# Performance work log

Hardware: AMD Instinct MI355X
Metric: run time of the kernel (lower is better)

The kernel has to match this reference:

```python
import jax, jax.numpy as jnp
import numpy as np

HEAD_COUNT = 16
EMBED_DIM = 2048
B, S = 2, 2048


def setup_inputs() -> dict:
    key = jax.random.key(0)
    k1, k2, k3, k4, k5 = jax.random.split(key, 5)
    keys = jax.random.normal(k1, (B, S, EMBED_DIM), dtype=jnp.float32)
    values = jax.random.normal(k2, (B, S, EMBED_DIM), dtype=jnp.float32)
    queries = jax.random.normal(k3, (B, S, EMBED_DIM), dtype=jnp.float32)
    # padding-style mask; guarantee at least one valid key per batch row
    attention_mask = jax.random.randint(k4, (B, S), 0, 2).astype(bool)
    attention_mask = attention_mask.at[:, 0].set(True)
    w_out = jax.random.normal(k5, (EMBED_DIM, EMBED_DIM), dtype=jnp.float32) * (EMBED_DIM ** -0.5)
    return {"keys": keys, "values": values, "queries": queries,
            "attention_mask": attention_mask, "w_out": w_out}


def reference(keys, values, queries, attention_mask, w_out):
    b, s, e = queries.shape
    h = HEAD_COUNT
    c = e // h  # head dim
    k = keys.reshape(b, s, h, c)
    v = values.reshape(b, s, h, c)
    q = queries.reshape(b, s, h, c) * (c ** -0.5)
    # [B,H,Q,K] scores + additive padding bias on key axis
    scores = jnp.einsum('bqhc,bkhc->bhqk', q, k)
    bias = jnp.where(attention_mask, 0.0, -jnp.inf)[:, None, None, :]
    weights = jax.nn.softmax(scores + bias, axis=-1)
    out = jnp.einsum('bhqk,bkhc->bqhc', weights, v).reshape(b, s, e)
    # nn.Linear(bias=False): y = x @ W^T
    return out @ w_out.T
```

## Files before the change

### kernel.cpp

```cpp
#include <hip/hip_runtime.h>
#include <hip/hip_bf16.h>
#include <math.h>

#define B_ 2
#define S_ 2048
#define E_ 2048
#define H_ 16
#define C_ 128

typedef __attribute__((ext_vector_type(8))) short s8v;
typedef __attribute__((ext_vector_type(4))) float f32x4;
typedef __attribute__((ext_vector_type(2))) unsigned u32x2;
typedef __attribute__((ext_vector_type(4))) unsigned u32x4;

#define MFMA16(a, b, c) __builtin_amdgcn_mfma_f32_16x16x32_bf16((a), (b), (c), 0, 0, 0)

__device__ __forceinline__ unsigned fbits(float f) {
    union { float f; unsigned u; } v{f};
    return v.u;
}
__device__ __forceinline__ short f2bfh(float f) {
    return (short)((fbits(f) + 0x8000u) >> 16);
}
__device__ __forceinline__ unsigned bfpack(float lo, float hi) {
    return __builtin_amdgcn_perm(fbits(hi) + 0x8000u, fbits(lo) + 0x8000u, 0x07060302u);
}

__device__ __forceinline__ float fexp2(float x) {
    float r;
    asm("v_exp_f32 %0, %1" : "=v"(r) : "v"(x));
    return r;
}
__device__ __forceinline__ float frcp(float x) {
    float r;
    asm("v_rcp_f32 %0, %1" : "=v"(r) : "v"(x));
    return r;
}

__device__ __forceinline__ void glds16(const void* g, void* l) {
    __builtin_amdgcn_global_load_lds(
        (const __attribute__((address_space(1))) void*)g,
        (__attribute__((address_space(3))) void*)l, 16, 0, 0);
}

template <bool DOK>
__global__ __launch_bounds__(256) void prep_kv(
    const float* __restrict__ K, const float* __restrict__ V,
    short* __restrict__ Kb, short* __restrict__ Vt)
{
    __shared__ __align__(16) short vt[C_][66];
    const int t  = threadIdx.x;
    const int s0 = blockIdx.x * 64;
    const int bh = blockIdx.y;
    const int b = bh >> 4, h = bh & 15;

    if (DOK) {
#pragma unroll
        for (int i = 0; i < 8; ++i) {
            int idx = t + i * 256;
            int s = idx >> 5, c4 = idx & 31;
            float4 v = *(const float4*)(K + ((size_t)(b * S_ + s0 + s)) * E_ + h * C_ + c4 * 4);
            u32x2 o = {bfpack(v.x, v.y), bfpack(v.z, v.w)};
            *(u32x2*)(Kb + ((size_t)(bh * S_ + s0 + s)) * C_ + c4 * 4) = o;
        }
    }
#pragma unroll
    for (int i = 0; i < 8; ++i) {
        int idx = t + i * 256;
        int r = idx >> 5, c4 = idx & 31;
        float4 v = *(const float4*)(V + ((size_t)(b * S_ + s0 + r)) * E_ + h * C_ + c4 * 4);
        vt[c4 * 4 + 0][r] = f2bfh(v.x);
        vt[c4 * 4 + 1][r] = f2bfh(v.y);
        vt[c4 * 4 + 2][r] = f2bfh(v.z);
        vt[c4 * 4 + 3][r] = f2bfh(v.w);
    }
    __syncthreads();
#pragma unroll
    for (int i = 0; i < 4; ++i) {
        int idx = t + i * 256;
        int c = idx >> 3, sc = idx & 7;
        *(s8v*)(Vt + ((size_t)(bh * C_ + c)) * S_ + s0 + sc * 8) = *(const s8v*)&vt[c][sc * 8];
    }
}

__global__ __launch_bounds__(256) void convw_kernel(
    const float* __restrict__ W, short* __restrict__ Wb)
{
    size_t i = ((size_t)blockIdx.x * 256 + threadIdx.x) * 8;
    float4 a = *(const float4*)(W + i);
    float4 b = *(const float4*)(W + i + 4);
    u32x4 o = {bfpack(a.x, a.y), bfpack(a.z, a.w), bfpack(b.x, b.y), bfpack(b.z, b.w)};
    *(u32x4*)(Wb + i) = o;
}

constexpr int QT = 256;
constexpr int KT = 64;
constexpr float M0 = 16.0f;

template <bool KBF16>
__global__ __launch_bounds__(512, 2) void attn_mfma(
    const short* __restrict__ Kb, const float* __restrict__ Kf,
    const float* __restrict__ Qp, const short* __restrict__ Vt,
    const int* __restrict__ maskp, short* __restrict__ Op)
{
    __shared__ __align__(16) short ks[2][KT * 128];
    __shared__ __align__(16) short vs[2][C_ * 64];
    __shared__ __align__(16) short ps[8][16][72];

    const int t = threadIdx.x;
    const int w = t >> 6, lane = t & 63;
    const int c15 = lane & 15, quad = lane >> 4;
    const int rbid = blockIdx.x;
    const int hb = (rbid & 7) + 8 * ((rbid >> 3) & 3);
    const int q0 = (rbid >> 5) * QT;
    const int h = hb & 15, b = hb >> 4;
    const int bh = b * H_ + h;

    const float qscale = 0.12751744458187936f;
    s8v qf[2][4];
#pragma unroll
    for (int mi = 0; mi < 2; ++mi) {
        const float* qrow = Qp + ((size_t)(b * S_ + q0 + w * 32 + mi * 16 + c15)) * E_ + h * C_;
#pragma unroll
        for (int kk = 0; kk < 4; ++kk) {
            const float* p = qrow + kk * 32 + quad * 8;
            float4 x0 = *(const float4*)p;
            float4 x1 = *(const float4*)(p + 4);
            u32x4 pk = {bfpack(x0.x * qscale, x0.y * qscale),
                        bfpack(x0.z * qscale, x0.w * qscale),
                        bfpack(x1.x * qscale, x1.y * qscale),
                        bfpack(x1.z * qscale, x1.w * qscale)};
            qf[mi][kk] = *(s8v*)&pk;
        }
    }

    s8v ones;
#pragma unroll
    for (int j = 0; j < 8; ++j) ones[j] = (short)0x3F80;

    f32x4 O[2][8], Ol[2];
#pragma unroll
    for (int mi = 0; mi < 2; ++mi) {
        Ol[mi] = (f32x4){0.f, 0.f, 0.f, 0.f};
#pragma unroll
        for (int ct = 0; ct < 8; ++ct) O[mi][ct] = (f32x4){0.f, 0.f, 0.f, 0.f};
    }

    const short* Kbh = Kb + (size_t)(bh * S_) * C_;
    const float* Kfh = Kf + (size_t)(b * S_) * E_ + h * C_;
    const short* Vbh = Vt + (size_t)(bh * C_) * S_;
    const int*   mptr = maskp + b * S_ + 4 * c15;

    int kgp[4], vgp[2];
#pragma unroll
    for (int kk = 0; kk < 4; ++kk) kgp[kk] = ((4 * kk + quad) ^ c15) * 8;
#pragma unroll
    for (int ks2 = 0; ks2 < 2; ++ks2) vgp[ks2] = ((4 * ks2 + quad) ^ (c15 & 7)) * 8;

    auto stage = [&](short* ksb, short* vsb, int k0) {
        const int r4 = lane >> 4, gp = lane & 15;
#pragma unroll
        for (int i = 0; i < 2; ++i) {
            int row = w * 8 + i * 4 + r4;
            int g = gp ^ ((row >> 2) & 15);
            glds16(Kbh + (size_t)(k0 + row) * C_ + g * 8, ksb + (w * 8 + i * 4) * 128);
        }
        const int cr = lane >> 3, gp7 = lane & 7;
#pragma unroll
        for (int i = 0; i < 2; ++i) {
            int c = w * 16 + i * 8 + cr;
            int g = gp7 ^ (c & 7);
            glds16(Vbh + (size_t)c * S_ + k0 + g * 8, vsb + (w * 16 + i * 8) * 64);
        }
    };

    auto compute = [&](const short* ksc, const short* vsc, int4 mv) {
        float bva[4] = {mv.x ? -M0 : -1e30f, mv.y ? -M0 : -1e30f,
                        mv.z ? -M0 : -1e30f, mv.w ? -M0 : -1e30f};
        f32x4 Sf[2][4];
        __builtin_amdgcn_s_setprio(1);
#pragma unroll
        for (int nt = 0; nt < 4; ++nt) {
            f32x4 s0 = (f32x4){bva[nt], bva[nt], bva[nt], bva[nt]};
            f32x4 s1 = s0;
            const short* krow = ksc + (4 * c15 + nt) * 128;
#pragma unroll
            for (int kk = 0; kk < 4; ++kk) {
                s8v bf = *(const s8v*)(krow + kgp[kk]);
                s0 = MFMA16(qf[0][kk], bf, s0);
                s1 = MFMA16(qf[1][kk], bf, s1);
            }
            Sf[0][nt] = s0; Sf[1][nt] = s1;
        }
        __builtin_amdgcn_s_setprio(0);

        s8v af[2][2];
#pragma unroll
        for (int mi = 0; mi < 2; ++mi) {
#pragma unroll
            for (int r = 0; r < 4; ++r) {
                float p0 = fexp2(Sf[mi][0][r]);
                float p1 = fexp2(Sf[mi][1][r]);
                float p2 = fexp2(Sf[mi][2][r]);
                float p3 = fexp2(Sf[mi][3][r]);
                u32x2 d = {bfpack(p0, p1), bfpack(p2, p3)};
                *(u32x2*)&ps[w][quad * 4 + r][4 * c15] = d;
            }
#pragma unroll
            for (int ks2 = 0; ks2 < 2; ++ks2)
                af[mi][ks2] = *(const s8v*)&ps[w][c15][ks2 * 32 + quad * 8];
        }

        __builtin_amdgcn_s_setprio(1);
#pragma unroll
        for (int ct = 0; ct < 8; ++ct) {
            const short* vrow = vsc + (ct * 16 + c15) * 64;
#pragma unroll
            for (int ks2 = 0; ks2 < 2; ++ks2) {
                s8v bf = *(const s8v*)(vrow + vgp[ks2]);
                O[0][ct] = MFMA16(af[0][ks2], bf, O[0][ct]);
                O[1][ct] = MFMA16(af[1][ks2], bf, O[1][ct]);
            }
        }
#pragma unroll
        for (int mi = 0; mi < 2; ++mi) {
            Ol[mi] = MFMA16(af[mi][0], ones, Ol[mi]);
            Ol[mi] = MFMA16(af[mi][1], ones, Ol[mi]);
        }
        __builtin_amdgcn_s_setprio(0);
    };

    if (KBF16) {
        stage(&ks[0][0], &vs[0][0], 0);
        int4 mcur = *(const int4*)mptr;
        __syncthreads();
#pragma unroll 1
        for (int k0 = 0; k0 < S_; k0 += 2 * KT) {
            stage(&ks[1][0], &vs[1][0], k0 + KT);
            int4 m1 = *(const int4*)(mptr + k0 + KT);
            compute(&ks[0][0], &vs[0][0], mcur);
            __syncthreads();

            int4 m2 = m1;
            if (k0 + 2 * KT < S_) {
                stage(&ks[0][0], &vs[0][0], k0 + 2 * KT);
                m2 = *(const int4*)(mptr + k0 + 2 * KT);
            }
            compute(&ks[1][0], &vs[1][0], m1);
            mcur = m2;
            __syncthreads();
        }
    } else {
#pragma unroll 1
        for (int k0 = 0; k0 < S_; k0 += KT) {
#pragma unroll
            for (int i = 0; i < 4; ++i) {
                int idx = t + i * 512;
                int r = idx >> 5, c4 = idx & 31;
                float4 kv = *(const float4*)(Kfh + (size_t)(k0 + r) * E_ + c4 * 4);
                u32x2 sv = {bfpack(kv.x, kv.y), bfpack(kv.z, kv.w)};
                int gpw = (c4 >> 1) ^ ((r >> 2) & 15);
                *(u32x2*)&ks[0][r * 128 + gpw * 8 + (c4 & 1) * 4] = sv;
            }
            {
                const int cr = lane >> 3, gp7 = lane & 7;
#pragma unroll
                for (int i = 0; i < 2; ++i) {
                    int c = w * 16 + i * 8 + cr;
                    int g = gp7 ^ (c & 7);
                    glds16(Vbh + (size_t)c * S_ + k0 + g * 8, &vs[0][(w * 16 + i * 8) * 64]);
                }
            }
            int4 mv = *(const int4*)(mptr + k0);
            __syncthreads();
            compute(&ks[0][0], &vs[0][0], mv);
            __syncthreads();
        }
    }

#pragma unroll
    for (int mi = 0; mi < 2; ++mi) {
        float inv[4];
#pragma unroll
        for (int r = 0; r < 4; ++r) inv[r] = frcp(Ol[mi][r]);
        size_t rbase = (size_t)(b * S_ + q0 + w * 32 + mi * 16 + quad * 4) * E_ + h * C_;
#pragma unroll
        for (int ct = 0; ct < 8; ++ct)
#pragma unroll
            for (int r = 0; r < 4; ++r)
                Op[rbase + (size_t)r * E_ + ct * 16 + c15] = f2bfh(O[mi][ct][r] * inv[r]);
    }
}

template <bool WBF16>
__global__ __launch_bounds__(512, 2) void proj_mfma(
    const short* __restrict__ X, const short* __restrict__ Wb,
    const float* __restrict__ Wf, float* __restrict__ Y)
{
    __shared__ __align__(16) short As[2][128 * 64];
    __shared__ __align__(16) short Bs[2][256 * 64];

    const int t = threadIdx.x;
    const int w = t >> 6, lane = t & 63;
    const int c15 = lane & 15, quad = lane >> 4;
    const int bm = blockIdx.x * 128, bn = blockIdx.y * 256;
    const int wm = (w >> 2) * 64, wn = (w & 3) * 64;

    f32x4 acc[4][4];
#pragma unroll
    for (int mi = 0; mi < 4; ++mi)
#pragma unroll
        for (int ni = 0; ni < 4; ++ni) acc[mi][ni] = (f32x4){0.f, 0.f, 0.f, 0.f};

    int agp[2];
#pragma unroll
    for (int kk = 0; kk < 2; ++kk) agp[kk] = ((4 * kk + quad) ^ (c15 & 7)) * 8;

    auto stageAB = [&](short* Ab, short* Bb, int k0) {
        const int r8 = lane >> 3, gp = lane & 7;
#pragma unroll
        for (int i = 0; i < 2; ++i) {
            int row = w * 16 + i * 8 + r8;
            int g = gp ^ (row & 7);
            glds16(X + (size_t)(bm + row) * E_ + k0 + g * 8, Ab + (w * 16 + i * 8) * 64);
        }
#pragma unroll
        for (int i = 0; i < 4; ++i) {
            int row = w * 32 + i * 8 + r8;
            int g = gp ^ (row & 7);
            glds16(Wb + (size_t)(bn + row) * E_ + k0 + g * 8, Bb + (w * 32 + i * 8) * 64);
        }
    };

    auto compute = [&](const short* Ab, const short* Bb) {
#pragma unroll
        for (int kk = 0; kk < 2; ++kk) {
            s8v a[4], bb[4];
#pragma unroll
            for (int mi = 0; mi < 4; ++mi)
                a[mi] = *(const s8v*)(Ab + (wm + mi * 16 + c15) * 64 + agp[kk]);
#pragma unroll
            for (int ni = 0; ni < 4; ++ni)
                bb[ni] = *(const s8v*)(Bb + (wn + ni * 16 + c15) * 64 + agp[kk]);
#pragma unroll
            for (int mi = 0; mi < 4; ++mi)
#pragma unroll
                for (int ni = 0; ni < 4; ++ni)
                    acc[mi][ni] = MFMA16(a[mi], bb[ni], acc[mi][ni]);
        }
    };

    if (WBF16) {
        stageAB(&As[0][0], &Bs[0][0], 0);
        __syncthreads();
#pragma unroll 1
        for (int k0 = 0; k0 < E_; k0 += 128) {
            stageAB(&As[1][0], &Bs[1][0], k0 + 64);
            compute(&As[0][0], &Bs[0][0]);
            __syncthreads();

            if (k0 + 128 < E_) stageAB(&As[0][0], &Bs[0][0], k0 + 128);
            compute(&As[1][0], &Bs[1][0]);
            __syncthreads();
        }
    } else {
#pragma unroll 1
        for (int k0 = 0; k0 < E_; k0 += 64) {
            {
                const int r8 = lane >> 3, gp = lane & 7;
#pragma unroll
                for (int i = 0; i < 2; ++i) {
                    int row = w * 16 + i * 8 + r8;
                    int g = gp ^ (row & 7);
                    glds16(X + (size_t)(bm + row) * E_ + k0 + g * 8, &As[0][(w * 16 + i * 8) * 64]);
                }
            }
#pragma unroll
            for (int i = 0; i < 8; ++i) {
                int idx = t + i * 512;
                int r = idx >> 4, c4 = idx & 15;
                float4 wv = *(const float4*)(Wf + (size_t)(bn + r) * E_ + k0 + c4 * 4);
                u32x2 sv = {bfpack(wv.x, wv.y), bfpack(wv.z, wv.w)};
                int gpw = (c4 >> 1) ^ (r & 7);
                *(u32x2*)&Bs[0][r * 64 + gpw * 8 + (c4 & 1) * 4] = sv;
            }
            __syncthreads();
            compute(&As[0][0], &Bs[0][0]);
            __syncthreads();
        }
    }

#pragma unroll
    for (int mi = 0; mi < 4; ++mi)
#pragma unroll
        for (int ni = 0; ni < 4; ++ni) {
            size_t rbase = (size_t)(bm + wm + mi * 16 + quad * 4) * E_ + bn + wn + ni * 16 + c15;
#pragma unroll
            for (int r = 0; r < 4; ++r) Y[rbase + (size_t)r * E_] = acc[mi][ni][r];
        }
}

extern "C" void kernel_launch(void* const* d_in, const int* in_sizes, int n_in,
                              void* d_out, int out_size, void* d_ws, size_t ws_size,
                              hipStream_t stream) {
    const float* keys    = (const float*)d_in[0];
    const float* values  = (const float*)d_in[1];
    const float* queries = (const float*)d_in[2];
    const int*   mask    = (const int*)d_in[3];
    const float* w_out   = (const float*)d_in[4];
    float* out = (float*)d_out;

    const size_t EL = (size_t)B_ * S_ * E_;
    short* ws  = (short*)d_ws;
    short* VtW = ws;
    short* Xb  = ws + EL;
    short* Kb  = ws + 2 * EL;
    short* Wb  = ws + 3 * EL;

    const bool hasK = ws_size >= (3 * EL) * 2;
    const bool hasW = ws_size >= (3 * EL + (size_t)E_ * E_) * 2;

    if (hasK)
        prep_kv<true><<<dim3(S_ / 64, B_ * H_), 256, 0, stream>>>(keys, values, Kb, VtW);
    else
        prep_kv<false><<<dim3(S_ / 64, B_ * H_), 256, 0, stream>>>(keys, values, Kb, VtW);
    if (hasW) convw_kernel<<<(E_ * E_ / 8) / 256, 256, 0, stream>>>(w_out, Wb);

    if (hasK)
        attn_mfma<true><<<dim3((S_ / QT) * H_ * B_), 512, 0, stream>>>(Kb, keys, queries, VtW, mask, Xb);
    else
        attn_mfma<false><<<dim3((S_ / QT) * H_ * B_), 512, 0, stream>>>(Kb, keys, queries, VtW, mask, Xb);

    if (hasW)
        proj_mfma<true><<<dim3((B_ * S_) / 128, E_ / 256), 512, 0, stream>>>(Xb, Wb, w_out, out);
    else
        proj_mfma<false><<<dim3((B_ * S_) / 128, E_ / 256), 512, 0, stream>>>(Xb, Wb, w_out, out);
}
```

Measured before the change: 269.7 us.

## Split-K projection GEMM across two wave groups with LDS reduction

The output projection now splits the K dimension between two groups of four waves, each accumulating a 64x128 sub-tile over half of K with its own LDS buffers. Partial sums are reduced through shared memory before the store. It also raises MFMA priority during compute and swaps the grid axes so neighbouring blocks share X rows. The B tile is now single-buffered with an extra barrier per step, and the accumulators double in size, which raises register pressure and may reduce occupancy under launch_bounds(512,2).

```diff
diff --git a/kernel.cpp b/kernel.cpp
--- a/kernel.cpp
+++ b/kernel.cpp
@@ -297,107 +297,125 @@
     const short* __restrict__ X, const short* __restrict__ Wb,
     const float* __restrict__ Wf, float* __restrict__ Y)
 {
-    __shared__ __align__(16) short As[2][128 * 64];
+    __shared__ __align__(16) short As[2][2][128 * 64];
     __shared__ __align__(16) short Bs[2][256 * 64];
 
     const int t = threadIdx.x;
     const int w = t >> 6, lane = t & 63;
     const int c15 = lane & 15, quad = lane >> 4;
-    const int bm = blockIdx.x * 128, bn = blockIdx.y * 256;
-    const int wm = (w >> 2) * 64, wn = (w & 3) * 64;
-
-    f32x4 acc[4][4];
+    const int g = w & 1, wi = w >> 1;
+    const int bn = blockIdx.x * 256, bm = blockIdx.y * 128;
+    const int wm = (wi >> 1) * 64, wn = (wi & 1) * 128;
+    const int kbase = g * (E_ / 2);
+
+    f32x4 acc[4][8];
 #pragma unroll
     for (int mi = 0; mi < 4; ++mi)
 #pragma unroll
-        for (int ni = 0; ni < 4; ++ni) acc[mi][ni] = (f32x4){0.f, 0.f, 0.f, 0.f};
+        for (int ni = 0; ni < 8; ++ni) acc[mi][ni] = (f32x4){0.f, 0.f, 0.f, 0.f};
 
     int agp[2];
 #pragma unroll
     for (int kk = 0; kk < 2; ++kk) agp[kk] = ((4 * kk + quad) ^ (c15 & 7)) * 8;
 
-    auto stageAB = [&](short* Ab, short* Bb, int k0) {
+    auto stageA = [&](int buf, int k0) {
         const int r8 = lane >> 3, gp = lane & 7;
-#pragma unroll
-        for (int i = 0; i < 2; ++i) {
-            int row = w * 16 + i * 8 + r8;
-            int g = gp ^ (row & 7);
-            glds16(X + (size_t)(bm + row) * E_ + k0 + g * 8, Ab + (w * 16 + i * 8) * 64);
-        }
+        short* Ab = &As[g][buf][0];
 #pragma unroll
         for (int i = 0; i < 4; ++i) {
-            int row = w * 32 + i * 8 + r8;
-            int g = gp ^ (row & 7);
-            glds16(Wb + (size_t)(bn + row) * E_ + k0 + g * 8, Bb + (w * 32 + i * 8) * 64);
-        }
-    };
-
-    auto compute = [&](const short* Ab, const short* Bb) {
+            int row = wi * 32 + i * 8 + r8;
+            int gg = gp ^ (row & 7);
+            glds16(X + (size_t)(bm + row) * E_ + kbase + k0 + gg * 8, Ab + (wi * 32 + i * 8) * 64);
+        }
+    };
+    auto stageB = [&](int k0) {
+        const int r8 = lane >> 3, gp = lane & 7;
+        short* Bb = &Bs[g][0];
+#pragma unroll
+        for (int i = 0; i < 8; ++i) {
+            int row = wi * 64 + i * 8 + r8;
+            int gg = gp ^ (row & 7);
+            glds16(Wb + (size_t)(bn + row) * E_ + kbase + k0 + gg * 8, Bb + (wi * 64 + i * 8) * 64);
+        }
+    };
+    auto convB = [&](int k0) {
+        const int tid4 = wi * 64 + lane;
+        short* Bb = &Bs[g][0];
+#pragma unroll
+        for (int i = 0; i < 16; ++i) {
+            int idx = tid4 + i * 256;
+            int r = idx >> 4, c4 = idx & 15;
+            float4 wv = *(const float4*)(Wf + (size_t)(bn + r) * E_ + kbase + k0 + c4 * 4);
+            u32x2 sv = {bfpack(wv.x, wv.y), bfpack(wv.z, wv.w)};
+            int gpw = (c4 >> 1) ^ (r & 7);
+            *(u32x2*)&Bb[r * 64 + gpw * 8 + (c4 & 1) * 4] = sv;
+        }
+    };
+
+    auto compute = [&](int buf) {
+        const short* Ab = &As[g][buf][0];
+        const short* Bb = &Bs[g][0];
+        __builtin_amdgcn_s_setprio(1);
 #pragma unroll
         for (int kk = 0; kk < 2; ++kk) {
-            s8v a[4], bb[4];
+            s8v a[4], bb[8];
 #pragma unroll
             for (int mi = 0; mi < 4; ++mi)
                 a[mi] = *(const s8v*)(Ab + (wm + mi * 16 + c15) * 64 + agp[kk]);
 #pragma unroll
-            for (int ni = 0; ni < 4; ++ni)
+            for (int ni = 0; ni < 8; ++ni)
                 bb[ni] = *(const s8v*)(Bb + (wn + ni * 16 + c15) * 64 + agp[kk]);
 #pragma unroll
             for (int mi = 0; mi < 4; ++mi)
 #pragma unroll
-                for (int ni = 0; ni < 4; ++ni)
+                for (int ni = 0; ni < 8; ++ni)
                     acc[mi][ni] = MFMA16(a[mi], bb[ni], acc[mi][ni]);
         }
-    };
-
-    if (WBF16) {
-        stageAB(&As[0][0], &Bs[0][0], 0);
+        __builtin_amdgcn_s_setprio(0);
+    };
+
+    stageA(0, 0);
+    if (WBF16) stageB(0); else convB(0);
+    __syncthreads();
+#pragma unroll 1
+    for (int j = 0; j < 16; ++j) {
+        if (j + 1 < 16) stageA((j + 1) & 1, (j + 1) * 64);
+        compute(j & 1);
         __syncthreads();
+        if (j + 1 < 16) { if (WBF16) stageB((j + 1) * 64); else convB((j + 1) * 64); }
+        __syncthreads();
+    }
+
+    float* mbuf = (float*)&As[0][0][0];
 #pragma unroll 1
-        for (int k0 = 0; k0 < E_; k0 += 128) {
-            stageAB(&As[1][0], &Bs[1][0], k0 + 64);
-            compute(&As[0][0], &Bs[0][0]);
-            __syncthreads();
-
-            if (k0 + 128 < E_) stageAB(&As[0][0], &Bs[0][0], k0 + 128);
-            compute(&As[1][0], &Bs[1][0]);
-            __syncthreads();
-        }
-    } else {
-#pragma unroll 1
-        for (int k0 = 0; k0 < E_; k0 += 64) {
-            {
-                const int r8 = lane >> 3, gp = lane & 7;
-#pragma unroll
-                for (int i = 0; i < 2; ++i) {
-                    int row = w * 16 + i * 8 + r8;
-                    int g = gp ^ (row & 7);
-                    glds16(X + (size_t)(bm + row) * E_ + k0 + g * 8, &As[0][(w * 16 + i * 8) * 64]);
-                }
-            }
-#pragma unroll
-            for (int i = 0; i < 8; ++i) {
-                int idx = t + i * 512;
-                int r = idx >> 4, c4 = idx & 15;
-                float4 wv = *(const float4*)(Wf + (size_t)(bn + r) * E_ + k0 + c4 * 4);
-                u32x2 sv = {bfpack(wv.x, wv.y), bfpack(wv.z, wv.w)};
-                int gpw = (c4 >> 1) ^ (r & 7);
-                *(u32x2*)&Bs[0][r * 64 + gpw * 8 + (c4 & 1) * 4] = sv;
-            }
-            __syncthreads();
-            compute(&As[0][0], &Bs[0][0]);
-            __syncthreads();
-        }
-    }
-
-#pragma unroll
-    for (int mi = 0; mi < 4; ++mi)
-#pragma unroll
-        for (int ni = 0; ni < 4; ++ni) {
-            size_t rbase = (size_t)(bm + wm + mi * 16 + quad * 4) * E_ + bn + wn + ni * 16 + c15;
-#pragma unroll
-            for (int r = 0; r < 4; ++r) Y[rbase + (size_t)r * E_] = acc[mi][ni][r];
-        }
+    for (int mi = 0; mi < 4; ++mi) {
+        if (g == 1) {
+#pragma unroll
+            for (int ni = 0; ni < 8; ++ni)
+#pragma unroll
+                for (int r = 0; r < 4; ++r)
+                    mbuf[((wi * 8 + ni) * 4 + r) * 64 + lane] = acc[mi][ni][r];
+        }
+        __syncthreads();
+        if (g == 0) {
+#pragma unroll
+            for (int ni = 0; ni < 8; ++ni)
+#pragma unroll
+                for (int r = 0; r < 4; ++r)
+                    acc[mi][ni][r] += mbuf[((wi * 8 + ni) * 4 + r) * 64 + lane];
+        }
+        __syncthreads();
+    }
+    if (g == 0) {
+#pragma unroll
+        for (int mi = 0; mi < 4; ++mi)
+#pragma unroll
+            for (int ni = 0; ni < 8; ++ni) {
+                size_t rbase = (size_t)(bm + wm + mi * 16 + quad * 4) * E_ + bn + wn + ni * 16 + c15;
+#pragma unroll
+                for (int r = 0; r < 4; ++r) Y[rbase + (size_t)r * E_] = acc[mi][ni][r];
+            }
+    }
 }
 
 extern "C" void kernel_launch(void* const* d_in, const int* in_sizes, int n_in,
@@ -432,7 +450,7 @@
         attn_mfma<false><<<dim3((S_ / QT) * H_ * B_), 512, 0, stream>>>(Kb, keys, queries, VtW, mask, Xb);
 
     if (hasW)
-        proj_mfma<true><<<dim3((B_ * S_) / 128, E_ / 256), 512, 0, stream>>>(Xb, Wb, w_out, out);
+        proj_mfma<true><<<dim3(E_ / 256, (B_ * S_) / 128), 512, 0, stream>>>(Xb, Wb, w_out, out);
     else
-        proj_mfma<false><<<dim3((B_ * S_) / 128, E_ / 256), 512, 0, stream>>>(Xb, Wb, w_out, out);
-}
+        proj_mfma<false><<<dim3(E_ / 256, (B_ * S_) / 128), 512, 0, stream>>>(Xb, Wb, w_out, out);
+}
```

Result: slower. 873.6 us (+223.9%).

## Fuse weight conversion into prep kernel and retile projection GEMM to 128x128

Applied to the files above, without the earlier changes.

Merges the fp32-to-bf16 weight conversion into the K/V prep kernel as extra grid rows, removing one kernel launch. The output projection GEMM moves from 256x128 tiles with 512 threads to 128x128 tiles with 256 threads, giving 512 blocks instead of 256. Block IDs are remapped so groups of 16 consecutive blocks share an M tile and span N, aiming for better L2 reuse and more even occupancy across CUs. The smaller tiles give less reuse per block in exchange for more parallelism.

```diff
diff --git a/kernel.cpp b/kernel.cpp
--- a/kernel.cpp
+++ b/kernel.cpp
@@ -43,13 +43,25 @@
         (__attribute__((address_space(3))) void*)l, 16, 0, 0);
 }
 
-template <bool DOK>
-__global__ __launch_bounds__(256) void prep_kv(
+template <bool DOK, bool DOW>
+__global__ __launch_bounds__(256) void prep_all(
     const float* __restrict__ K, const float* __restrict__ V,
-    short* __restrict__ Kb, short* __restrict__ Vt)
+    const float* __restrict__ W,
+    short* __restrict__ Kb, short* __restrict__ Vt, short* __restrict__ Wb)
 {
     __shared__ __align__(16) short vt[C_][66];
-    const int t  = threadIdx.x;
+    const int t = threadIdx.x;
+
+    if (DOW && blockIdx.y >= 32) {
+        int cid = (blockIdx.y - 32) * 32 + blockIdx.x;
+        size_t i = ((size_t)cid * 256 + t) * 8;
+        float4 a = *(const float4*)(W + i);
+        float4 b = *(const float4*)(W + i + 4);
+        u32x4 o = {bfpack(a.x, a.y), bfpack(a.z, a.w), bfpack(b.x, b.y), bfpack(b.z, b.w)};
+        *(u32x4*)(Wb + i) = o;
+        return;
+    }
+
     const int s0 = blockIdx.x * 64;
     const int bh = blockIdx.y;
     const int b = bh >> 4, h = bh & 15;
@@ -81,16 +93,6 @@
         int c = idx >> 3, sc = idx & 7;
         *(s8v*)(Vt + ((size_t)(bh * C_ + c)) * S_ + s0 + sc * 8) = *(const s8v*)&vt[c][sc * 8];
     }
-}
-
-__global__ __launch_bounds__(256) void convw_kernel(
-    const float* __restrict__ W, short* __restrict__ Wb)
-{
-    size_t i = ((size_t)blockIdx.x * 256 + threadIdx.x) * 8;
-    float4 a = *(const float4*)(W + i);
-    float4 b = *(const float4*)(W + i + 4);
-    u32x4 o = {bfpack(a.x, a.y), bfpack(a.z, a.w), bfpack(b.x, b.y), bfpack(b.z, b.w)};
-    *(u32x4*)(Wb + i) = o;
 }
 
 constexpr int QT = 256;
@@ -293,18 +295,20 @@
 }
 
 template <bool WBF16>
-__global__ __launch_bounds__(512, 2) void proj_mfma(
+__global__ __launch_bounds__(256, 2) void proj_mfma(
     const short* __restrict__ X, const short* __restrict__ Wb,
     const float* __restrict__ Wf, float* __restrict__ Y)
 {
     __shared__ __align__(16) short As[2][128 * 64];
-    __shared__ __align__(16) short Bs[2][256 * 64];
+    __shared__ __align__(16) short Bs[2][128 * 64];
 
     const int t = threadIdx.x;
     const int w = t >> 6, lane = t & 63;
     const int c15 = lane & 15, quad = lane >> 4;
-    const int bm = blockIdx.x * 128, bn = blockIdx.y * 256;
-    const int wm = (w >> 2) * 64, wn = (w & 3) * 64;
+    const int pid = blockIdx.x;
+    const int bn = ((pid & 7) + 8 * ((pid >> 3) & 1)) * 128;
+    const int bm = (pid >> 4) * 128;
+    const int wm = (w >> 1) * 64, wn = (w & 1) * 64;
 
     f32x4 acc[4][4];
 #pragma unroll
@@ -318,16 +322,11 @@
 
     auto stageAB = [&](short* Ab, short* Bb, int k0) {
         const int r8 = lane >> 3, gp = lane & 7;
-#pragma unroll
-        for (int i = 0; i < 2; ++i) {
-            int row = w * 16 + i * 8 + r8;
-            int g = gp ^ (row & 7);
-            glds16(X + (size_t)(bm + row) * E_ + k0 + g * 8, Ab + (w * 16 + i * 8) * 64);
-        }
 #pragma unroll
         for (int i = 0; i < 4; ++i) {
             int row = w * 32 + i * 8 + r8;
             int g = gp ^ (row & 7);
+            glds16(X + (size_t)(bm + row) * E_ + k0 + g * 8, Ab + (w * 32 + i * 8) * 64);
             glds16(Wb + (size_t)(bn + row) * E_ + k0 + g * 8, Bb + (w * 32 + i * 8) * 64);
         }
     };
@@ -369,15 +368,15 @@
             {
                 const int r8 = lane >> 3, gp = lane & 7;
 #pragma unroll
-                for (int i = 0; i < 2; ++i) {
-                    int row = w * 16 + i * 8 + r8;
+                for (int i = 0; i < 4; ++i) {
+                    int row = w * 32 + i * 8 + r8;
                     int g = gp ^ (row & 7);
-                    glds16(X + (size_t)(bm + row) * E_ + k0 + g * 8, &As[0][(w * 16 + i * 8) * 64]);
+                    glds16(X + (size_t)(bm + row) * E_ + k0 + g * 8, &As[0][(w * 32 + i * 8) * 64]);
                 }
             }
 #pragma unroll
             for (int i = 0; i < 8; ++i) {
-                int idx = t + i * 512;
+                int idx = t + i * 256;
                 int r = idx >> 4, c4 = idx & 15;
                 float4 wv = *(const float4*)(Wf + (size_t)(bn + r) * E_ + k0 + c4 * 4);
                 u32x2 sv = {bfpack(wv.x, wv.y), bfpack(wv.z, wv.w)};
@@ -420,11 +419,12 @@
     const bool hasK = ws_size >= (3 * EL) * 2;
     const bool hasW = ws_size >= (3 * EL + (size_t)E_ * E_) * 2;
 
-    if (hasK)
-        prep_kv<true><<<dim3(S_ / 64, B_ * H_), 256, 0, stream>>>(keys, values, Kb, VtW);
+    if (hasK && hasW)
+        prep_all<true, true><<<dim3(S_ / 64, 96), 256, 0, stream>>>(keys, values, w_out, Kb, VtW, Wb);
+    else if (hasK)
+        prep_all<true, false><<<dim3(S_ / 64, 32), 256, 0, stream>>>(keys, values, w_out, Kb, VtW, Wb);
     else
-        prep_kv<false><<<dim3(S_ / 64, B_ * H_), 256, 0, stream>>>(keys, values, Kb, VtW);
-    if (hasW) convw_kernel<<<(E_ * E_ / 8) / 256, 256, 0, stream>>>(w_out, Wb);
+        prep_all<false, false><<<dim3(S_ / 64, 32), 256, 0, stream>>>(keys, values, w_out, Kb, VtW, Wb);
 
     if (hasK)
         attn_mfma<true><<<dim3((S_ / QT) * H_ * B_), 512, 0, stream>>>(Kb, keys, queries, VtW, mask, Xb);
@@ -432,7 +432,7 @@
         attn_mfma<false><<<dim3((S_ / QT) * H_ * B_), 512, 0, stream>>>(Kb, keys, queries, VtW, mask, Xb);
 
     if (hasW)
-        proj_mfma<true><<<dim3((B_ * S_) / 128, E_ / 256), 512, 0, stream>>>(Xb, Wb, w_out, out);
+        proj_mfma<true><<<dim3(512), 256, 0, stream>>>(Xb, Wb, w_out, out);
     else
-        proj_mfma<false><<<dim3((B_ * S_) / 128, E_ / 256), 512, 0, stream>>>(Xb, Wb, w_out, out);
-}
+        proj_mfma<false><<<dim3(512), 256, 0, stream>>>(Xb, Wb, w_out, out);
+}
```

Result: no change. 270.1 us (+0.1%).
